# Kernel optimization log

Hardware: AMD Instinct MI355X
Metric: run time of the kernel (lower is better)

## Reference

```python
import jax, jax.numpy as jnp
import numpy as np

B, N, E = 4, 1024, 8192
NF_IN, NF_H, NF_OUT = 32, 128, 3


def _lin(key, fan_in, fan_out):
    k1, k2 = jax.random.split(key)
    bound = 1.0 / np.sqrt(fan_in)
    W = jax.random.uniform(k1, (fan_in, fan_out), jnp.float32, -bound, bound)
    b = jax.random.uniform(k2, (fan_out,), jnp.float32, -bound, bound)
    return W, b


def setup_inputs() -> dict:
    key = jax.random.key(0)
    ks = jax.random.split(key, 16)
    x = jax.random.normal(ks[0], (B, N, NF_IN), jnp.float32)
    # One-hot receiver/sender relation matrices [B, E, N]
    recv = jax.random.randint(ks[1], (B, E), 0, N)
    send = jax.random.randint(ks[2], (B, E), 0, N)
    Rr = jax.nn.one_hot(recv, N, dtype=jnp.float32)
    Rs = jax.nn.one_hot(send, N, dtype=jnp.float32)
    neW0, neb0 = _lin(ks[3], NF_IN, NF_H)
    neW1, neb1 = _lin(ks[4], NF_H, NF_H)
    neW2, neb2 = _lin(ks[5], NF_H, NF_H)
    eeW0, eeb0 = _lin(ks[6], NF_IN * 2, NF_H)
    eeW1, eeb1 = _lin(ks[7], NF_H, NF_H)
    eeW2, eeb2 = _lin(ks[8], NF_H, NF_H)
    npW, npb = _lin(ks[9], NF_H * 2, NF_H)
    epW, epb = _lin(ks[10], NF_H * 3, NF_H)
    ppW0, ppb0 = _lin(ks[11], NF_H * 2, NF_H)
    ppW1, ppb1 = _lin(ks[12], NF_H, NF_H)
    ppW2, ppb2 = _lin(ks[13], NF_H, NF_OUT)
    return dict(x=x, Rr=Rr, Rs=Rs, pstep=2,
                neW0=neW0, neb0=neb0, neW1=neW1, neb1=neb1, neW2=neW2, neb2=neb2,
                eeW0=eeW0, eeb0=eeb0, eeW1=eeW1, eeb1=eeb1, eeW2=eeW2, eeb2=eeb2,
                npW=npW, npb=npb, epW=epW, epb=epb,
                ppW0=ppW0, ppb0=ppb0, ppW1=ppW1, ppb1=ppb1, ppW2=ppW2, ppb2=ppb2)


def _encoder(x, W0, b0, W1, b1, W2, b2):
    # Linear->ReLU x3 (ReLU after last layer too)
    h = jax.nn.relu(x @ W0 + b0)
    h = jax.nn.relu(h @ W1 + b1)
    return jax.nn.relu(h @ W2 + b2)


def _predictor(x, W0, b0, W1, b1, W2, b2):
    h = jax.nn.relu(x @ W0 + b0)
    h = jax.nn.relu(h @ W1 + b1)
    return h @ W2 + b2


def reference(x, Rr, Rs, pstep,
              neW0, neb0, neW1, neb1, neW2, neb2,
              eeW0, eeb0, eeW1, eeb1, eeW2, eeb2,
              npW, npb, epW, epb,
              ppW0, ppb0, ppW1, ppb1, ppW2, ppb2):
    node_encode = _encoder(x, neW0, neb0, neW1, neb1, neW2, neb2)  # [B,N,H]
    node_effect = node_encode
    x_r = jnp.einsum('ben,bnf->bef', Rr, x)  # gather receiver features
    x_s = jnp.einsum('ben,bnf->bef', Rs, x)  # gather sender features
    edge_encode = _encoder(jnp.concatenate([x_r, x_s], -1),
                           eeW0, eeb0, eeW1, eeb1, eeW2, eeb2)  # [B,E,H]
    for _ in range(pstep):
        ne_r = jnp.einsum('ben,bnh->beh', Rr, node_effect)
        ne_s = jnp.einsum('ben,bnh->beh', Rs, node_effect)
        edge_in = jnp.concatenate([edge_encode, ne_r, ne_s], -1)  # [B,E,3H]
        edge_effect = jax.nn.relu(edge_in @ epW + epb)  # [B,E,H]
        agg = jnp.einsum('ben,beh->bnh', Rr, edge_effect)  # scatter-add to receivers
        node_in = jnp.concatenate([node_encode, agg], -1)  # [B,N,2H]
        node_effect = jax.nn.relu(node_in @ npW + npb + node_effect)  # residual
    node_reps = _predictor(jnp.concatenate([node_encode, node_effect], -1),
                           ppW0, ppb0, ppW1, ppb1, ppW2, ppb2)  # [B,N,out]
    return node_reps
```

## Files before the change

### kernel.cpp

```cpp
#include <hip/hip_runtime.h>
#include <hip/hip_bf16.h>


typedef unsigned short u16;
typedef __attribute__((ext_vector_type(8))) __bf16 bf16x8;
typedef __attribute__((ext_vector_type(4))) float f32x4;

#define N_    1024
#define BN    4096
#define BE    32768
#define LOG_E 13
#define H_    128
#define LSTR  132

__device__ __forceinline__ u16 f2bf(float f) {
    __bf16 h = (__bf16)f;
    return __builtin_bit_cast(u16, h);
}

__device__ __forceinline__ bf16x8 cvt8(float4 f0, float4 f1) {
    bf16x8 a;
    a[0] = (__bf16)f0.x; a[1] = (__bf16)f0.y; a[2] = (__bf16)f0.z; a[3] = (__bf16)f0.w;
    a[4] = (__bf16)f1.x; a[5] = (__bf16)f1.y; a[6] = (__bf16)f1.z; a[7] = (__bf16)f1.w;
    return a;
}

__device__ __forceinline__ bf16x8 a_from_f32(const float* p) {
    float4 f0 = *(const float4*)p;
    float4 f1 = *(const float4*)(p + 4);
    return cvt8(f0, f1);
}

__device__ __forceinline__ bf16x8 a_from_lds(const float* lds, int m, int quad, int c) {
    return a_from_f32(lds + m * LSTR + c * 32 + quad * 8);
}

__device__ __forceinline__ void mm8(const u16* __restrict__ Wf, int c, bf16x8 a,
                                    f32x4* acc, int lane) {
    const u16* wp = Wf + ((size_t)c * 8) * 64 * 8;
    #pragma unroll
    for (int nt = 0; nt < 8; ++nt) {
        bf16x8 bw = *(const bf16x8*)(wp + (size_t)(nt * 64 + lane) * 8);
        acc[nt] = __builtin_amdgcn_mfma_f32_16x16x32_bf16(a, bw, acc[nt], 0, 0, 0);
    }
}

__device__ __forceinline__ void zacc(f32x4* acc) {
    #pragma unroll
    for (int t = 0; t < 8; ++t) acc[t] = (f32x4){0.f, 0.f, 0.f, 0.f};
}

__device__ __forceinline__ void epi_to_lds(float* lds, const f32x4* acc,
                                           const float* __restrict__ bias,
                                           int quad, int m) {
    #pragma unroll
    for (int nt = 0; nt < 8; ++nt) {
        float bv = bias[nt * 16 + m];
        #pragma unroll
        for (int i = 0; i < 4; ++i)
            lds[(quad * 4 + i) * LSTR + nt * 16 + m] = fmaxf(acc[nt][i] + bv, 0.f);
    }
}

struct WDesc { const float* src; u16* dst; int K; };
struct WPack { WDesc d[10]; };

__global__ __launch_bounds__(256) void k_wprep(WPack P, float* __restrict__ agg) {
    if (blockIdx.y == 10) {
        int i = blockIdx.x * 256 + threadIdx.x;
        for (int t = i; t < BN * H_ / 4; t += 192 * 256)
            ((float4*)agg)[t] = make_float4(0.f, 0.f, 0.f, 0.f);
        return;
    }
    WDesc d = P.d[blockIdx.y];
    int i = blockIdx.x * 256 + threadIdx.x;
    if (i >= d.K * 128) return;
    int j    = i & 7;
    int lane = (i >> 3) & 63;
    int nt   = (i >> 9) & 7;
    int c    = i >> 12;
    int k = c * 32 + (lane >> 4) * 8 + j;
    int n = nt * 16 + (lane & 15);
    d.dst[i] = f2bf(d.src[k * 128 + n]);
}

__global__ __launch_bounds__(256) void k_extract(const float* __restrict__ Rr,
                                                 const float* __restrict__ Rs,
                                                 int* __restrict__ recv,
                                                 int* __restrict__ send) {
    int wave = threadIdx.x >> 6, lane = threadIdx.x & 63;
    int g = blockIdx.x * 4 + wave;
    const float* src;
    int* dst;
    if (g < BE) { src = Rr + (size_t)g * N_;        dst = recv + g; }
    else        { src = Rs + (size_t)(g - BE) * N_; dst = send + (g - BE); }
    int idx = 0;
    bool done = false;
    #pragma unroll
    for (int it = 0; it < 4; ++it) {
        if (!done) {
            int base = it * 256 + lane * 4;
            float4 v = *(const float4*)(src + base);
            int found = -1;
            if      (v.x != 0.f) found = base;
            else if (v.y != 0.f) found = base + 1;
            else if (v.z != 0.f) found = base + 2;
            else if (v.w != 0.f) found = base + 3;
            unsigned long long msk = __ballot(found >= 0);
            if (msk) {
                int sl = __ffsll((long long)msk) - 1;
                idx = __shfl(found, sl, 64);
                done = true;
            }
        }
    }
    if (lane == 0) *dst = idx;
}

__global__ __launch_bounds__(64) void k_node3(
    const float* __restrict__ x,
    const u16* __restrict__ W0, const float* __restrict__ b0,
    const u16* __restrict__ W1, const float* __restrict__ b1,
    const u16* __restrict__ W2, const float* __restrict__ b2,
    float* __restrict__ nenc)
{
    __shared__ float lds[2][16 * LSTR];
    int lane = threadIdx.x, m = lane & 15, quad = lane >> 4;
    int row16 = blockIdx.x * 16;
    f32x4 acc[8];

    zacc(acc);
    mm8(W0, 0, a_from_f32(x + (size_t)(row16 + m) * 32 + quad * 8), acc, lane);
    epi_to_lds(lds[0], acc, b0, quad, m);

    zacc(acc);
    #pragma unroll
    for (int c = 0; c < 4; ++c) mm8(W1, c, a_from_lds(lds[0], m, quad, c), acc, lane);
    epi_to_lds(lds[1], acc, b1, quad, m);

    zacc(acc);
    #pragma unroll
    for (int c = 0; c < 4; ++c) mm8(W2, c, a_from_lds(lds[1], m, quad, c), acc, lane);
    epi_to_lds(lds[0], acc, b2, quad, m);

    #pragma unroll
    for (int t = 0; t < 32; ++t) {
        int flat = t * 64 + lane;
        int r = flat >> 7, col = flat & 127;
        nenc[(size_t)(row16 + r) * H_ + col] = lds[0][r * LSTR + col];
    }
}

__global__ __launch_bounds__(64) void k_edge3(
    const float* __restrict__ x,
    const int* __restrict__ recv, const int* __restrict__ send,
    const u16* __restrict__ W0, const float* __restrict__ b0,
    const u16* __restrict__ W1, const float* __restrict__ b1,
    const u16* __restrict__ W2, const float* __restrict__ b2,
    u16* __restrict__ eenc)
{
    __shared__ float lds[2][16 * LSTR];
    int lane = threadIdx.x, m = lane & 15, quad = lane >> 4;
    int row16 = blockIdx.x * 16;
    int e = row16 + m, b = e >> LOG_E;
    long rr = (long)b * N_ + recv[e];
    long rs = (long)b * N_ + send[e];
    f32x4 acc[8];

    zacc(acc);
    mm8(W0, 0, a_from_f32(x + rr * 32 + quad * 8), acc, lane);
    mm8(W0, 1, a_from_f32(x + rs * 32 + quad * 8), acc, lane);
    epi_to_lds(lds[0], acc, b0, quad, m);

    zacc(acc);
    #pragma unroll
    for (int c = 0; c < 4; ++c) mm8(W1, c, a_from_lds(lds[0], m, quad, c), acc, lane);
    epi_to_lds(lds[1], acc, b1, quad, m);

    zacc(acc);
    #pragma unroll
    for (int c = 0; c < 4; ++c) mm8(W2, c, a_from_lds(lds[1], m, quad, c), acc, lane);
    epi_to_lds(lds[0], acc, b2, quad, m);

    #pragma unroll
    for (int t = 0; t < 16; ++t) {
        int r = t, col = lane * 2;
        u16 lo = f2bf(lds[0][r * LSTR + col]);
        u16 hi = f2bf(lds[0][r * LSTR + col + 1]);
        *(unsigned*)(eenc + (size_t)(row16 + r) * H_ + col) =
            (unsigned)lo | ((unsigned)hi << 16);
    }
}

__global__ __launch_bounds__(64) void k_eprop(
    const u16* __restrict__ eenc, const float* __restrict__ eff,
    const int* __restrict__ recv, const int* __restrict__ send,
    const u16* __restrict__ Wf, const float* __restrict__ bias,
    float* __restrict__ agg)
{
    int lane = threadIdx.x, m = lane & 15, quad = lane >> 4;
    int row16 = blockIdx.x * 16;
    int e = row16 + m, b = e >> LOG_E;
    long rr = (long)b * N_ + recv[e];
    long rs = (long)b * N_ + send[e];
    f32x4 acc[8];
    zacc(acc);

    #pragma unroll
    for (int c = 0; c < 4; ++c)
        mm8(Wf, c, *(const bf16x8*)(eenc + (size_t)e * H_ + c * 32 + quad * 8), acc, lane);
    #pragma unroll
    for (int c = 0; c < 4; ++c)
        mm8(Wf, 4 + c, a_from_f32(eff + rr * H_ + c * 32 + quad * 8), acc, lane);
    #pragma unroll
    for (int c = 0; c < 4; ++c)
        mm8(Wf, 8 + c, a_from_f32(eff + rs * H_ + c * 32 + quad * 8), acc, lane);

    size_t tgt[4];
    #pragma unroll
    for (int i = 0; i < 4; ++i) {
        int r = row16 + quad * 4 + i;
        tgt[i] = ((size_t)(r >> LOG_E) * N_ + recv[r]) * H_;
    }
    #pragma unroll
    for (int nt = 0; nt < 8; ++nt) {
        int col = nt * 16 + m;
        float bv = bias[col];
        #pragma unroll
        for (int i = 0; i < 4; ++i)
            atomicAdd(agg + tgt[i] + col, fmaxf(acc[nt][i] + bv, 0.f));
    }
}

__global__ __launch_bounds__(64) void k_nprop(
    const float* __restrict__ nenc, float* __restrict__ agg,
    const float* __restrict__ eff,
    const u16* __restrict__ Wf, const float* __restrict__ bias,
    float* __restrict__ nout)
{
    int lane = threadIdx.x, m = lane & 15, quad = lane >> 4;
    int row16 = blockIdx.x * 16;
    int row = row16 + m;
    f32x4 acc[8];
    zacc(acc);

    #pragma unroll
    for (int c = 0; c < 4; ++c)
        mm8(Wf, c, a_from_f32(nenc + (size_t)row * H_ + c * 32 + quad * 8), acc, lane);
    #pragma unroll
    for (int c = 0; c < 4; ++c)
        mm8(Wf, 4 + c, a_from_f32(agg + (size_t)row * H_ + c * 32 + quad * 8), acc, lane);

    #pragma unroll
    for (int nt = 0; nt < 8; ++nt) {
        int col = nt * 16 + m;
        float bv = bias[col];
        #pragma unroll
        for (int i = 0; i < 4; ++i) {
            int r = row16 + quad * 4 + i;
            float v = fmaxf(acc[nt][i] + bv + eff[(size_t)r * H_ + col], 0.f);
            nout[(size_t)r * H_ + col] = v;
            agg[(size_t)r * H_ + col] = 0.f;
        }
    }
}

__global__ __launch_bounds__(64) void k_pred(
    const float* __restrict__ nenc, const float* __restrict__ eff,
    const u16* __restrict__ W0, const float* __restrict__ b0,
    const u16* __restrict__ W1, const float* __restrict__ b1,
    const float* __restrict__ W2, const float* __restrict__ b2,
    float* __restrict__ out)
{
    __shared__ float lds[2][16 * LSTR];
    int lane = threadIdx.x, m = lane & 15, quad = lane >> 4;
    int row16 = blockIdx.x * 16;
    int row = row16 + m;
    f32x4 acc[8];

    zacc(acc);
    #pragma unroll
    for (int c = 0; c < 4; ++c)
        mm8(W0, c, a_from_f32(nenc + (size_t)row * H_ + c * 32 + quad * 8), acc, lane);
    #pragma unroll
    for (int c = 0; c < 4; ++c)
        mm8(W0, 4 + c, a_from_f32(eff + (size_t)row * H_ + c * 32 + quad * 8), acc, lane);
    epi_to_lds(lds[0], acc, b0, quad, m);

    zacc(acc);
    #pragma unroll
    for (int c = 0; c < 4; ++c) mm8(W1, c, a_from_lds(lds[0], m, quad, c), acc, lane);
    epi_to_lds(lds[1], acc, b1, quad, m);

    int r = lane & 15, col = lane >> 4;
    if (col < 3) {
        float s = 0.f;
        #pragma unroll 8
        for (int k = 0; k < 128; ++k)
            s += lds[1][r * LSTR + k] * W2[k * 3 + col];
        out[(size_t)(row16 + r) * 3 + col] = s + b2[col];
    }
}

extern "C" void kernel_launch(void* const* d_in, const int* in_sizes, int n_in,
                              void* d_out, int out_size, void* d_ws, size_t ws_size,
                              hipStream_t stream) {
    (void)in_sizes; (void)n_in; (void)out_size; (void)ws_size;

    const float* x    = (const float*)d_in[0];
    const float* Rr   = (const float*)d_in[1];
    const float* Rs   = (const float*)d_in[2];
    const float* neW0 = (const float*)d_in[4];  const float* neb0 = (const float*)d_in[5];
    const float* neW1 = (const float*)d_in[6];  const float* neb1 = (const float*)d_in[7];
    const float* neW2 = (const float*)d_in[8];  const float* neb2 = (const float*)d_in[9];
    const float* eeW0 = (const float*)d_in[10]; const float* eeb0 = (const float*)d_in[11];
    const float* eeW1 = (const float*)d_in[12]; const float* eeb1 = (const float*)d_in[13];
    const float* eeW2 = (const float*)d_in[14]; const float* eeb2 = (const float*)d_in[15];
    const float* npW  = (const float*)d_in[16]; const float* npb  = (const float*)d_in[17];
    const float* epW  = (const float*)d_in[18]; const float* epb  = (const float*)d_in[19];
    const float* ppW0 = (const float*)d_in[20]; const float* ppb0 = (const float*)d_in[21];
    const float* ppW1 = (const float*)d_in[22]; const float* ppb1 = (const float*)d_in[23];
    const float* ppW2 = (const float*)d_in[24]; const float* ppb2 = (const float*)d_in[25];

    char* ws = (char*)d_ws;
    size_t off = 0;
    auto alloc = [&](size_t bytes) -> char* {
        char* p = ws + off;
        off += (bytes + 255) & ~(size_t)255;
        return p;
    };

    u16* f_neW0 = (u16*)alloc(32  * 128 * 2);
    u16* f_neW1 = (u16*)alloc(128 * 128 * 2);
    u16* f_neW2 = (u16*)alloc(128 * 128 * 2);
    u16* f_eeW0 = (u16*)alloc(64  * 128 * 2);
    u16* f_eeW1 = (u16*)alloc(128 * 128 * 2);
    u16* f_eeW2 = (u16*)alloc(128 * 128 * 2);
    u16* f_epW  = (u16*)alloc(384 * 128 * 2);
    u16* f_npW  = (u16*)alloc(256 * 128 * 2);
    u16* f_ppW0 = (u16*)alloc(256 * 128 * 2);
    u16* f_ppW1 = (u16*)alloc(128 * 128 * 2);
    int*   recv = (int*)alloc(BE * 4);
    int*   send = (int*)alloc(BE * 4);
    float* nenc = (float*)alloc((size_t)BN * H_ * 4);
    float* nef1 = (float*)alloc((size_t)BN * H_ * 4);
    float* nef2 = (float*)alloc((size_t)BN * H_ * 4);
    float* agg  = (float*)alloc((size_t)BN * H_ * 4);
    u16*   eenc = (u16*)alloc((size_t)BE * H_ * 2);

    WPack P;
    P.d[0] = {neW0, f_neW0, 32};
    P.d[1] = {neW1, f_neW1, 128};
    P.d[2] = {neW2, f_neW2, 128};
    P.d[3] = {eeW0, f_eeW0, 64};
    P.d[4] = {eeW1, f_eeW1, 128};
    P.d[5] = {eeW2, f_eeW2, 128};
    P.d[6] = {epW,  f_epW,  384};
    P.d[7] = {npW,  f_npW,  256};
    P.d[8] = {ppW0, f_ppW0, 256};
    P.d[9] = {ppW1, f_ppW1, 128};
    k_wprep<<<dim3(192, 11), 256, 0, stream>>>(P, agg);

    k_extract<<<(2 * BE) / 4, 256, 0, stream>>>(Rr, Rs, recv, send);

    k_node3<<<BN / 16, 64, 0, stream>>>(x, f_neW0, neb0, f_neW1, neb1, f_neW2, neb2, nenc);
    k_edge3<<<BE / 16, 64, 0, stream>>>(x, recv, send,
                                        f_eeW0, eeb0, f_eeW1, eeb1, f_eeW2, eeb2, eenc);

    k_eprop<<<BE / 16, 64, 0, stream>>>(eenc, nenc, recv, send, f_epW, epb, agg);
    k_nprop<<<BN / 16, 64, 0, stream>>>(nenc, agg, nenc, f_npW, npb, nef1);
    k_eprop<<<BE / 16, 64, 0, stream>>>(eenc, nef1, recv, send, f_epW, epb, agg);
    k_nprop<<<BN / 16, 64, 0, stream>>>(nenc, agg, nef1, f_npW, npb, nef2);

    k_pred<<<BN / 16, 64, 0, stream>>>(nenc, nef2, f_ppW0, ppb0, f_ppW1, ppb1,
                                       ppW2, ppb2, (float*)d_out);
}
```

Baseline: 397.0 us.

## Process two edge tiles per wave, store bf16 node copies, split node kernels across waves

The edge kernels (encoder and propagation) now handle 32 edges per wave, so each weight fragment loaded from memory feeds two MFMAs. The node kernels also write bf16 copies of their outputs, which lets the edge gather read half the bytes and skip per-fragment conversion. Node, node-propagation and predictor kernels split the output columns across 2 or 4 waves, adding barriers, to get more parallelism out of the small node count. In exchange there are extra bf16 buffers and writes, higher register pressure from doubled accumulators, and fewer edge blocks.

```diff
diff --git a/kernel.cpp b/kernel.cpp
--- a/kernel.cpp
+++ b/kernel.cpp
@@ -31,34 +31,76 @@
     return cvt8(f0, f1);
 }
 
-__device__ __forceinline__ bf16x8 a_from_lds(const float* lds, int m, int quad, int c) {
-    return a_from_f32(lds + m * LSTR + c * 32 + quad * 8);
-}
-
-__device__ __forceinline__ void mm8(const u16* __restrict__ Wf, int c, bf16x8 a,
-                                    f32x4* acc, int lane) {
+__device__ __forceinline__ bf16x8 a_from_lds(const float* lds, int r, int quad, int c) {
+    return a_from_f32(lds + r * LSTR + c * 32 + quad * 8);
+}
+
+__device__ __forceinline__ void mm8x2(const u16* __restrict__ Wf, int c,
+                                      bf16x8 a0, bf16x8 a1,
+                                      f32x4 (*acc)[8], int lane) {
     const u16* wp = Wf + ((size_t)c * 8) * 64 * 8;
     #pragma unroll
     for (int nt = 0; nt < 8; ++nt) {
         bf16x8 bw = *(const bf16x8*)(wp + (size_t)(nt * 64 + lane) * 8);
+        acc[0][nt] = __builtin_amdgcn_mfma_f32_16x16x32_bf16(a0, bw, acc[0][nt], 0, 0, 0);
+        acc[1][nt] = __builtin_amdgcn_mfma_f32_16x16x32_bf16(a1, bw, acc[1][nt], 0, 0, 0);
+    }
+}
+
+__device__ __forceinline__ void mm4(const u16* __restrict__ Wf, int c, int ntb,
+                                    bf16x8 a, f32x4* acc, int lane) {
+    const u16* wp = Wf + ((size_t)c * 8) * 64 * 8;
+    #pragma unroll
+    for (int nt = 0; nt < 4; ++nt) {
+        bf16x8 bw = *(const bf16x8*)(wp + (size_t)((ntb + nt) * 64 + lane) * 8);
         acc[nt] = __builtin_amdgcn_mfma_f32_16x16x32_bf16(a, bw, acc[nt], 0, 0, 0);
     }
 }
 
-__device__ __forceinline__ void zacc(f32x4* acc) {
+__device__ __forceinline__ void mm2(const u16* __restrict__ Wf, int c, int ntb,
+                                    bf16x8 a, f32x4* acc, int lane) {
+    const u16* wp = Wf + ((size_t)c * 8) * 64 * 8;
+    #pragma unroll
+    for (int nt = 0; nt < 2; ++nt) {
+        bf16x8 bw = *(const bf16x8*)(wp + (size_t)((ntb + nt) * 64 + lane) * 8);
+        acc[nt] = __builtin_amdgcn_mfma_f32_16x16x32_bf16(a, bw, acc[nt], 0, 0, 0);
+    }
+}
+
+__device__ __forceinline__ void zacc8(f32x4* acc) {
     #pragma unroll
     for (int t = 0; t < 8; ++t) acc[t] = (f32x4){0.f, 0.f, 0.f, 0.f};
 }
-
-__device__ __forceinline__ void epi_to_lds(float* lds, const f32x4* acc,
+__device__ __forceinline__ void zacc4(f32x4* acc) {
+    #pragma unroll
+    for (int t = 0; t < 4; ++t) acc[t] = (f32x4){0.f, 0.f, 0.f, 0.f};
+}
+
+__device__ __forceinline__ void epi8x2_lds(float* lds, f32x4 (*acc)[8],
                                            const float* __restrict__ bias,
                                            int quad, int m) {
     #pragma unroll
-    for (int nt = 0; nt < 8; ++nt) {
-        float bv = bias[nt * 16 + m];
+    for (int t = 0; t < 2; ++t)
+        #pragma unroll
+        for (int nt = 0; nt < 8; ++nt) {
+            float bv = bias[nt * 16 + m];
+            #pragma unroll
+            for (int i = 0; i < 4; ++i)
+                lds[(t * 16 + quad * 4 + i) * LSTR + nt * 16 + m] =
+                    fmaxf(acc[t][nt][i] + bv, 0.f);
+        }
+}
+
+__device__ __forceinline__ void epi4_lds(float* lds, const f32x4* acc,
+                                         const float* __restrict__ bias,
+                                         int quad, int m, int ntb) {
+    #pragma unroll
+    for (int nt = 0; nt < 4; ++nt) {
+        int col = (ntb + nt) * 16 + m;
+        float bv = bias[col];
         #pragma unroll
         for (int i = 0; i < 4; ++i)
-            lds[(quad * 4 + i) * LSTR + nt * 16 + m] = fmaxf(acc[nt][i] + bv, 0.f);
+            lds[(quad * 4 + i) * LSTR + col] = fmaxf(acc[nt][i] + bv, 0.f);
     }
 }
 
@@ -117,37 +159,48 @@
     if (lane == 0) *dst = idx;
 }
 
-__global__ __launch_bounds__(64) void k_node3(
+__global__ __launch_bounds__(128) void k_node3(
     const float* __restrict__ x,
     const u16* __restrict__ W0, const float* __restrict__ b0,
     const u16* __restrict__ W1, const float* __restrict__ b1,
     const u16* __restrict__ W2, const float* __restrict__ b2,
-    float* __restrict__ nenc)
+    float* __restrict__ nenc_f, u16* __restrict__ nenc_bf)
 {
     __shared__ float lds[2][16 * LSTR];
-    int lane = threadIdx.x, m = lane & 15, quad = lane >> 4;
-    int row16 = blockIdx.x * 16;
-    f32x4 acc[8];
-
-    zacc(acc);
-    mm8(W0, 0, a_from_f32(x + (size_t)(row16 + m) * 32 + quad * 8), acc, lane);
-    epi_to_lds(lds[0], acc, b0, quad, m);
-
-    zacc(acc);
-    #pragma unroll
-    for (int c = 0; c < 4; ++c) mm8(W1, c, a_from_lds(lds[0], m, quad, c), acc, lane);
-    epi_to_lds(lds[1], acc, b1, quad, m);
-
-    zacc(acc);
-    #pragma unroll
-    for (int c = 0; c < 4; ++c) mm8(W2, c, a_from_lds(lds[1], m, quad, c), acc, lane);
-    epi_to_lds(lds[0], acc, b2, quad, m);
-
-    #pragma unroll
-    for (int t = 0; t < 32; ++t) {
-        int flat = t * 64 + lane;
-        int r = flat >> 7, col = flat & 127;
-        nenc[(size_t)(row16 + r) * H_ + col] = lds[0][r * LSTR + col];
+    int tid = threadIdx.x, lane = tid & 63, w = tid >> 6;
+    int m = lane & 15, quad = lane >> 4;
+    int row16 = blockIdx.x * 16, ntb = w * 4;
+    f32x4 acc[4];
+
+    zacc4(acc);
+    mm4(W0, 0, ntb, a_from_f32(x + (size_t)(row16 + m) * 32 + quad * 8), acc, lane);
+    epi4_lds(lds[0], acc, b0, quad, m, ntb);
+    __syncthreads();
+
+    zacc4(acc);
+    #pragma unroll
+    for (int c = 0; c < 4; ++c) mm4(W1, c, ntb, a_from_lds(lds[0], m, quad, c), acc, lane);
+    epi4_lds(lds[1], acc, b1, quad, m, ntb);
+    __syncthreads();
+
+    zacc4(acc);
+    #pragma unroll
+    for (int c = 0; c < 4; ++c) mm4(W2, c, ntb, a_from_lds(lds[1], m, quad, c), acc, lane);
+    epi4_lds(lds[0], acc, b2, quad, m, ntb);
+    __syncthreads();
+
+    #pragma unroll
+    for (int t = 0; t < 16; ++t) {
+        int flat = t * 128 + tid, r = flat >> 7, col = flat & 127;
+        nenc_f[(size_t)(row16 + r) * H_ + col] = lds[0][r * LSTR + col];
+    }
+    #pragma unroll
+    for (int t = 0; t < 8; ++t) {
+        int p = t * 128 + tid, r = p >> 6, c2 = (p & 63) * 2;
+        u16 lo = f2bf(lds[0][r * LSTR + c2]);
+        u16 hi = f2bf(lds[0][r * LSTR + c2 + 1]);
+        *(unsigned*)(nenc_bf + (size_t)(row16 + r) * H_ + c2) =
+            (unsigned)lo | ((unsigned)hi << 16);
     }
 }
 
@@ -159,146 +212,177 @@
     const u16* __restrict__ W2, const float* __restrict__ b2,
     u16* __restrict__ eenc)
 {
-    __shared__ float lds[2][16 * LSTR];
+    __shared__ float lds[2][32 * LSTR];
     int lane = threadIdx.x, m = lane & 15, quad = lane >> 4;
-    int row16 = blockIdx.x * 16;
-    int e = row16 + m, b = e >> LOG_E;
-    long rr = (long)b * N_ + recv[e];
-    long rs = (long)b * N_ + send[e];
-    f32x4 acc[8];
-
-    zacc(acc);
-    mm8(W0, 0, a_from_f32(x + rr * 32 + quad * 8), acc, lane);
-    mm8(W0, 1, a_from_f32(x + rs * 32 + quad * 8), acc, lane);
-    epi_to_lds(lds[0], acc, b0, quad, m);
-
-    zacc(acc);
-    #pragma unroll
-    for (int c = 0; c < 4; ++c) mm8(W1, c, a_from_lds(lds[0], m, quad, c), acc, lane);
-    epi_to_lds(lds[1], acc, b1, quad, m);
-
-    zacc(acc);
-    #pragma unroll
-    for (int c = 0; c < 4; ++c) mm8(W2, c, a_from_lds(lds[1], m, quad, c), acc, lane);
-    epi_to_lds(lds[0], acc, b2, quad, m);
-
-    #pragma unroll
-    for (int t = 0; t < 16; ++t) {
-        int r = t, col = lane * 2;
-        u16 lo = f2bf(lds[0][r * LSTR + col]);
-        u16 hi = f2bf(lds[0][r * LSTR + col + 1]);
-        *(unsigned*)(eenc + (size_t)(row16 + r) * H_ + col) =
+    int row32 = blockIdx.x * 32;
+    int e0 = row32 + m, e1 = e0 + 16;
+    long base0 = (long)(e0 >> LOG_E) * N_, base1 = (long)(e1 >> LOG_E) * N_;
+    long rr0 = base0 + recv[e0], rs0 = base0 + send[e0];
+    long rr1 = base1 + recv[e1], rs1 = base1 + send[e1];
+    f32x4 acc[2][8];
+
+    zacc8(acc[0]); zacc8(acc[1]);
+    mm8x2(W0, 0, a_from_f32(x + rr0 * 32 + quad * 8),
+                 a_from_f32(x + rr1 * 32 + quad * 8), acc, lane);
+    mm8x2(W0, 1, a_from_f32(x + rs0 * 32 + quad * 8),
+                 a_from_f32(x + rs1 * 32 + quad * 8), acc, lane);
+    epi8x2_lds(lds[0], acc, b0, quad, m);
+
+    zacc8(acc[0]); zacc8(acc[1]);
+    #pragma unroll
+    for (int c = 0; c < 4; ++c)
+        mm8x2(W1, c, a_from_lds(lds[0], m, quad, c),
+                     a_from_lds(lds[0], m + 16, quad, c), acc, lane);
+    epi8x2_lds(lds[1], acc, b1, quad, m);
+
+    zacc8(acc[0]); zacc8(acc[1]);
+    #pragma unroll
+    for (int c = 0; c < 4; ++c)
+        mm8x2(W2, c, a_from_lds(lds[1], m, quad, c),
+                     a_from_lds(lds[1], m + 16, quad, c), acc, lane);
+    epi8x2_lds(lds[0], acc, b2, quad, m);
+
+    #pragma unroll
+    for (int t = 0; t < 32; ++t) {
+        int col = lane * 2;
+        u16 lo = f2bf(lds[0][t * LSTR + col]);
+        u16 hi = f2bf(lds[0][t * LSTR + col + 1]);
+        *(unsigned*)(eenc + (size_t)(row32 + t) * H_ + col) =
             (unsigned)lo | ((unsigned)hi << 16);
     }
 }
 
 __global__ __launch_bounds__(64) void k_eprop(
-    const u16* __restrict__ eenc, const float* __restrict__ eff,
+    const u16* __restrict__ eenc, const u16* __restrict__ eff_bf,
     const int* __restrict__ recv, const int* __restrict__ send,
     const u16* __restrict__ Wf, const float* __restrict__ bias,
     float* __restrict__ agg)
 {
     int lane = threadIdx.x, m = lane & 15, quad = lane >> 4;
-    int row16 = blockIdx.x * 16;
-    int e = row16 + m, b = e >> LOG_E;
-    long rr = (long)b * N_ + recv[e];
-    long rs = (long)b * N_ + send[e];
-    f32x4 acc[8];
-    zacc(acc);
-
-    #pragma unroll
-    for (int c = 0; c < 4; ++c)
-        mm8(Wf, c, *(const bf16x8*)(eenc + (size_t)e * H_ + c * 32 + quad * 8), acc, lane);
-    #pragma unroll
-    for (int c = 0; c < 4; ++c)
-        mm8(Wf, 4 + c, a_from_f32(eff + rr * H_ + c * 32 + quad * 8), acc, lane);
-    #pragma unroll
-    for (int c = 0; c < 4; ++c)
-        mm8(Wf, 8 + c, a_from_f32(eff + rs * H_ + c * 32 + quad * 8), acc, lane);
-
-    size_t tgt[4];
-    #pragma unroll
-    for (int i = 0; i < 4; ++i) {
-        int r = row16 + quad * 4 + i;
-        tgt[i] = ((size_t)(r >> LOG_E) * N_ + recv[r]) * H_;
-    }
-    #pragma unroll
-    for (int nt = 0; nt < 8; ++nt) {
-        int col = nt * 16 + m;
-        float bv = bias[col];
+    int row32 = blockIdx.x * 32;
+    int e0 = row32 + m, e1 = e0 + 16;
+    long rr0 = ((long)(e0 >> LOG_E) * N_ + recv[e0]) * H_;
+    long rs0 = ((long)(e0 >> LOG_E) * N_ + send[e0]) * H_;
+    long rr1 = ((long)(e1 >> LOG_E) * N_ + recv[e1]) * H_;
+    long rs1 = ((long)(e1 >> LOG_E) * N_ + send[e1]) * H_;
+    f32x4 acc[2][8];
+    zacc8(acc[0]); zacc8(acc[1]);
+
+    #pragma unroll
+    for (int c = 0; c < 4; ++c)
+        mm8x2(Wf, c,
+              *(const bf16x8*)(eenc + (size_t)e0 * H_ + c * 32 + quad * 8),
+              *(const bf16x8*)(eenc + (size_t)e1 * H_ + c * 32 + quad * 8), acc, lane);
+    #pragma unroll
+    for (int c = 0; c < 4; ++c)
+        mm8x2(Wf, 4 + c,
+              *(const bf16x8*)(eff_bf + rr0 + c * 32 + quad * 8),
+              *(const bf16x8*)(eff_bf + rr1 + c * 32 + quad * 8), acc, lane);
+    #pragma unroll
+    for (int c = 0; c < 4; ++c)
+        mm8x2(Wf, 8 + c,
+              *(const bf16x8*)(eff_bf + rs0 + c * 32 + quad * 8),
+              *(const bf16x8*)(eff_bf + rs1 + c * 32 + quad * 8), acc, lane);
+
+    size_t tgt[2][4];
+    #pragma unroll
+    for (int t = 0; t < 2; ++t)
         #pragma unroll
-        for (int i = 0; i < 4; ++i)
-            atomicAdd(agg + tgt[i] + col, fmaxf(acc[nt][i] + bv, 0.f));
-    }
-}
-
-__global__ __launch_bounds__(64) void k_nprop(
-    const float* __restrict__ nenc, float* __restrict__ agg,
-    const float* __restrict__ eff,
+        for (int i = 0; i < 4; ++i) {
+            int r = row32 + t * 16 + quad * 4 + i;
+            tgt[t][i] = ((size_t)(r >> LOG_E) * N_ + recv[r]) * H_;
+        }
+    #pragma unroll
+    for (int t = 0; t < 2; ++t)
+        #pragma unroll
+        for (int nt = 0; nt < 8; ++nt) {
+            int col = nt * 16 + m;
+            float bv = bias[col];
+            #pragma unroll
+            for (int i = 0; i < 4; ++i)
+                atomicAdd(agg + tgt[t][i] + col, fmaxf(acc[t][nt][i] + bv, 0.f));
+        }
+}
+
+__global__ __launch_bounds__(256) void k_nprop(
+    const u16* __restrict__ nenc_bf, float* __restrict__ agg,
+    const float* __restrict__ eff_f,
     const u16* __restrict__ Wf, const float* __restrict__ bias,
-    float* __restrict__ nout)
+    float* __restrict__ nout_f, u16* __restrict__ nout_bf)
 {
-    int lane = threadIdx.x, m = lane & 15, quad = lane >> 4;
-    int row16 = blockIdx.x * 16;
-    int row = row16 + m;
-    f32x4 acc[8];
-    zacc(acc);
-
-    #pragma unroll
-    for (int c = 0; c < 4; ++c)
-        mm8(Wf, c, a_from_f32(nenc + (size_t)row * H_ + c * 32 + quad * 8), acc, lane);
-    #pragma unroll
-    for (int c = 0; c < 4; ++c)
-        mm8(Wf, 4 + c, a_from_f32(agg + (size_t)row * H_ + c * 32 + quad * 8), acc, lane);
-
-    #pragma unroll
-    for (int nt = 0; nt < 8; ++nt) {
-        int col = nt * 16 + m;
+    int tid = threadIdx.x, lane = tid & 63, w = tid >> 6;
+    int m = lane & 15, quad = lane >> 4;
+    int row16 = blockIdx.x * 16, row = row16 + m, ntb = w * 2;
+    f32x4 acc[2];
+    acc[0] = (f32x4){0.f, 0.f, 0.f, 0.f};
+    acc[1] = (f32x4){0.f, 0.f, 0.f, 0.f};
+
+    #pragma unroll
+    for (int c = 0; c < 4; ++c)
+        mm2(Wf, c, ntb,
+            *(const bf16x8*)(nenc_bf + (size_t)row * H_ + c * 32 + quad * 8), acc, lane);
+    #pragma unroll
+    for (int c = 0; c < 4; ++c)
+        mm2(Wf, 4 + c, ntb,
+            a_from_f32(agg + (size_t)row * H_ + c * 32 + quad * 8), acc, lane);
+
+    __syncthreads();
+
+    #pragma unroll
+    for (int nt = 0; nt < 2; ++nt) {
+        int col = (ntb + nt) * 16 + m;
         float bv = bias[col];
         #pragma unroll
         for (int i = 0; i < 4; ++i) {
             int r = row16 + quad * 4 + i;
-            float v = fmaxf(acc[nt][i] + bv + eff[(size_t)r * H_ + col], 0.f);
-            nout[(size_t)r * H_ + col] = v;
+            float v = fmaxf(acc[nt][i] + bv + eff_f[(size_t)r * H_ + col], 0.f);
+            nout_f[(size_t)r * H_ + col] = v;
+            nout_bf[(size_t)r * H_ + col] = f2bf(v);
             agg[(size_t)r * H_ + col] = 0.f;
         }
     }
 }
 
-__global__ __launch_bounds__(64) void k_pred(
-    const float* __restrict__ nenc, const float* __restrict__ eff,
+__global__ __launch_bounds__(128) void k_pred(
+    const u16* __restrict__ nenc_bf, const u16* __restrict__ eff_bf,
     const u16* __restrict__ W0, const float* __restrict__ b0,
     const u16* __restrict__ W1, const float* __restrict__ b1,
     const float* __restrict__ W2, const float* __restrict__ b2,
     float* __restrict__ out)
 {
     __shared__ float lds[2][16 * LSTR];
-    int lane = threadIdx.x, m = lane & 15, quad = lane >> 4;
-    int row16 = blockIdx.x * 16;
-    int row = row16 + m;
-    f32x4 acc[8];
-
-    zacc(acc);
-    #pragma unroll
-    for (int c = 0; c < 4; ++c)
-        mm8(W0, c, a_from_f32(nenc + (size_t)row * H_ + c * 32 + quad * 8), acc, lane);
-    #pragma unroll
-    for (int c = 0; c < 4; ++c)
-        mm8(W0, 4 + c, a_from_f32(eff + (size_t)row * H_ + c * 32 + quad * 8), acc, lane);
-    epi_to_lds(lds[0], acc, b0, quad, m);
-
-    zacc(acc);
-    #pragma unroll
-    for (int c = 0; c < 4; ++c) mm8(W1, c, a_from_lds(lds[0], m, quad, c), acc, lane);
-    epi_to_lds(lds[1], acc, b1, quad, m);
-
-    int r = lane & 15, col = lane >> 4;
-    if (col < 3) {
-        float s = 0.f;
-        #pragma unroll 8
-        for (int k = 0; k < 128; ++k)
-            s += lds[1][r * LSTR + k] * W2[k * 3 + col];
-        out[(size_t)(row16 + r) * 3 + col] = s + b2[col];
+    int tid = threadIdx.x, lane = tid & 63, w = tid >> 6;
+    int m = lane & 15, quad = lane >> 4;
+    int row16 = blockIdx.x * 16, row = row16 + m, ntb = w * 4;
+    f32x4 acc[4];
+
+    zacc4(acc);
+    #pragma unroll
+    for (int c = 0; c < 4; ++c)
+        mm4(W0, c, ntb,
+            *(const bf16x8*)(nenc_bf + (size_t)row * H_ + c * 32 + quad * 8), acc, lane);
+    #pragma unroll
+    for (int c = 0; c < 4; ++c)
+        mm4(W0, 4 + c, ntb,
+            *(const bf16x8*)(eff_bf + (size_t)row * H_ + c * 32 + quad * 8), acc, lane);
+    epi4_lds(lds[0], acc, b0, quad, m, ntb);
+    __syncthreads();
+
+    zacc4(acc);
+    #pragma unroll
+    for (int c = 0; c < 4; ++c) mm4(W1, c, ntb, a_from_lds(lds[0], m, quad, c), acc, lane);
+    epi4_lds(lds[1], acc, b1, quad, m, ntb);
+    __syncthreads();
+
+    if (w == 0) {
+        int r = lane & 15, col = lane >> 4;
+        if (col < 3) {
+            float s = 0.f;
+            #pragma unroll 8
+            for (int k = 0; k < 128; ++k)
+                s += lds[1][r * LSTR + k] * W2[k * 3 + col];
+            out[(size_t)(row16 + r) * 3 + col] = s + b2[col];
+        }
     }
 }
 
@@ -342,9 +426,12 @@
     u16* f_ppW1 = (u16*)alloc(128 * 128 * 2);
     int*   recv = (int*)alloc(BE * 4);
     int*   send = (int*)alloc(BE * 4);
-    float* nenc = (float*)alloc((size_t)BN * H_ * 4);
-    float* nef1 = (float*)alloc((size_t)BN * H_ * 4);
-    float* nef2 = (float*)alloc((size_t)BN * H_ * 4);
+    float* nenc_f  = (float*)alloc((size_t)BN * H_ * 4);
+    u16*   nenc_bf = (u16*)alloc((size_t)BN * H_ * 2);
+    float* nef1_f  = (float*)alloc((size_t)BN * H_ * 4);
+    u16*   nef1_bf = (u16*)alloc((size_t)BN * H_ * 2);
+    float* nef2_f  = (float*)alloc((size_t)BN * H_ * 4);
+    u16*   nef2_bf = (u16*)alloc((size_t)BN * H_ * 2);
     float* agg  = (float*)alloc((size_t)BN * H_ * 4);
     u16*   eenc = (u16*)alloc((size_t)BE * H_ * 2);
 
@@ -363,15 +450,16 @@
 
     k_extract<<<(2 * BE) / 4, 256, 0, stream>>>(Rr, Rs, recv, send);
 
-    k_node3<<<BN / 16, 64, 0, stream>>>(x, f_neW0, neb0, f_neW1, neb1, f_neW2, neb2, nenc);
-    k_edge3<<<BE / 16, 64, 0, stream>>>(x, recv, send,
+    k_node3<<<BN / 16, 128, 0, stream>>>(x, f_neW0, neb0, f_neW1, neb1, f_neW2, neb2,
+                                         nenc_f, nenc_bf);
+    k_edge3<<<BE / 32, 64, 0, stream>>>(x, recv, send,
                                         f_eeW0, eeb0, f_eeW1, eeb1, f_eeW2, eeb2, eenc);
 
-    k_eprop<<<BE / 16, 64, 0, stream>>>(eenc, nenc, recv, send, f_epW, epb, agg);
-    k_nprop<<<BN / 16, 64, 0, stream>>>(nenc, agg, nenc, f_npW, npb, nef1);
-    k_eprop<<<BE / 16, 64, 0, stream>>>(eenc, nef1, recv, send, f_epW, epb, agg);
-    k_nprop<<<BN / 16, 64, 0, stream>>>(nenc, agg, nef1, f_npW, npb, nef2);
-
-    k_pred<<<BN / 16, 64, 0, stream>>>(nenc, nef2, f_ppW0, ppb0, f_ppW1, ppb1,
-                                       ppW2, ppb2, (float*)d_out);
-}
+    k_eprop<<<BE / 32, 64, 0, stream>>>(eenc, nenc_bf, recv, send, f_epW, epb, agg);
+    k_nprop<<<BN / 16, 256, 0, stream>>>(nenc_bf, agg, nenc_f, f_npW, npb, nef1_f, nef1_bf);
+    k_eprop<<<BE / 32, 64, 0, stream>>>(eenc, nef1_bf, recv, send, f_epW, epb, agg);
+    k_nprop<<<BN / 16, 256, 0, stream>>>(nenc_bf, agg, nef1_f, f_npW, npb, nef2_f, nef2_bf);
+
+    k_pred<<<BN / 16, 128, 0, stream>>>(nenc_bf, nef2_bf, f_ppW0, ppb0, f_ppW1, ppb1,
+                                        ppW2, ppb2, (float*)d_out);
+}
```

New measurement: 415.8 us. +4.7%, slower.
